# Optimization experiments

Hardware: AMD Instinct MI355X
Metric: run time of the kernel (lower is better)

Reference implementation:

```python
import jax, jax.numpy as jnp
import numpy as np

VOCAB, EMB, HID, SEQ, BATCH, NLAYERS = 10000, 512, 1024, 128, 64, 2


def setup_inputs() -> dict:
    key = jax.random.key(0)
    ks = jax.random.split(key, 10)
    b = 1.0 / np.sqrt(HID)
    U = lambda k, shape, a: jax.random.uniform(k, shape, jnp.float32, -a, a)
    return {
        "inputs": jax.random.randint(ks[0], (SEQ, BATCH), 0, VOCAB, dtype=jnp.int32),
        "hidden": jnp.zeros((NLAYERS, BATCH, HID), jnp.float32),
        "emb": U(ks[1], (VOCAB, EMB), 0.1),
        # layer 0: Linear(emb+hid -> hid), split into input/recurrent parts
        "W0x": U(ks[2], (HID, EMB), b),
        "W0h": U(ks[3], (HID, HID), b),
        "b0": U(ks[4], (HID,), b),
        # layer 1: Linear(2*hid -> hid)
        "W1x": U(ks[5], (HID, HID), b),
        "W1h": U(ks[6], (HID, HID), b),
        "b1": U(ks[7], (HID,), b),
        "Wout": U(ks[8], (VOCAB, HID), 0.1),
        "bout": jnp.zeros((VOCAB,), jnp.float32),
    }


def reference(inputs, hidden, emb, W0x, W0h, b0, W1x, W1h, b1, Wout, bout):
    # Stacked tanh RNN; dropout is identity since dp_keep_prob = 1.0.
    def step(h, tok):
        x = emb[tok]  # (B, E)
        h0 = jnp.tanh(x @ W0x.T + h[0] @ W0h.T + b0)   # (B, H)
        h1 = jnp.tanh(h0 @ W1x.T + h[1] @ W1h.T + b1)  # (B, H)
        logits = h1 @ Wout.T + bout                     # (B, V)
        return jnp.stack([h0, h1]), logits

    final_hidden, logits = jax.lax.scan(step, hidden, inputs)
    return logits, final_hidden
```

## Files before the change

kernel.cpp:

```cpp
#include <hip/hip_runtime.h>
#include <hip/hip_bf16.h>

#define SEQ 128
#define BATCH 64
#define EMB 512
#define HID 1024
#define VOCAB 10000
#define NPAD 10240
#define MROWS 8192
#define BH (BATCH * HID)

typedef unsigned short u16;
typedef unsigned int u32;
typedef __attribute__((ext_vector_type(4))) float f32x4;
typedef __attribute__((ext_vector_type(8))) short short8;
typedef __attribute__((ext_vector_type(8))) __bf16 bf16x8;

__device__ __forceinline__ u16 f2bf(float f) {
  u32 u = __builtin_bit_cast(u32, f);
  u = (u + 0x7fffu + ((u >> 16) & 1u)) >> 16;
  return (u16)u;
}
__device__ __forceinline__ float bf2f(u16 h) {
  u32 u = ((u32)h) << 16;
  return __builtin_bit_cast(float, u);
}
__device__ __forceinline__ f32x4 mfma_bf16(short8 a, short8 b, f32x4 c) {
  return __builtin_amdgcn_mfma_f32_16x16x32_bf16(
      __builtin_bit_cast(bf16x8, a), __builtin_bit_cast(bf16x8, b), c, 0, 0, 0);
}
__device__ __forceinline__ void gload16(const u16* g, u16* l) {
  __builtin_amdgcn_global_load_lds(
      (__attribute__((address_space(1))) void*)g,
      (__attribute__((address_space(3))) void*)l, 16, 0, 0);
}

__global__ void k_cvt(const float* __restrict__ s, u16* __restrict__ d, int n) {
  int i = blockIdx.x * 256 + threadIdx.x;
  if (i < n) d[i] = f2bf(s[i]);
}
__global__ void k_cvt_wout(const float* __restrict__ s, u16* __restrict__ d) {
  int i = blockIdx.x * 256 + threadIdx.x;
  if (i < NPAD * HID) {
    int row = i >> 10;
    d[i] = (row < VOCAB) ? f2bf(s[i]) : (u16)0;
  }
}
__global__ void k_gather(const int* __restrict__ toks, const float* __restrict__ emb,
                         u16* __restrict__ X) {
  int i = blockIdx.x * 256 + threadIdx.x;
  if (i < MROWS * EMB) {
    int r = i >> 9, e = i & 511;
    X[i] = f2bf(emb[(size_t)toks[r] * EMB + e]);
  }
}
__global__ void k_zero(int* __restrict__ p, int n) {
  int i = blockIdx.x * 256 + threadIdx.x;
  if (i < n) p[i] = 0;
}

__global__ __launch_bounds__(256) void k_gemm(const u16* __restrict__ A, const u16* __restrict__ B,
                                              float* __restrict__ C, int K, int ldc, int nvalid,
                                              const float* __restrict__ bias) {
  __shared__ u16 As[128 * 32];
  __shared__ u16 Bs[128 * 32];
  const int tid = threadIdx.x, lane = tid & 63, wid = tid >> 6;
  const int wm = wid >> 1, wn = wid & 1;
  const int bm = blockIdx.x, bn = blockIdx.y;
  const int r4 = tid >> 2;
  const int csw = (((tid & 3) ^ ((r4 >> 1) & 3))) * 8;
  f32x4 acc[4][4] = {};
  const u16* Ab = A + (size_t)bm * 128 * K;
  const u16* Bb = B + (size_t)bn * 128 * K;
  const int nkt = K >> 5;
  for (int kt = 0; kt < nkt; ++kt) {
    const int k0 = kt * 32;
    __syncthreads();
#pragma unroll
    for (int c = 0; c < 2; ++c) {
      gload16(Ab + (size_t)(c * 64 + r4) * K + k0 + csw, &As[c * 2048 + wid * 512]);
      gload16(Bb + (size_t)(c * 64 + r4) * K + k0 + csw, &Bs[c * 2048 + wid * 512]);
    }
    __syncthreads();
    short8 af[4], bf[4];
    const int rr = lane & 15, g = lane >> 4;
    const int kq2 = ((g ^ ((rr >> 1) & 3))) * 8;
#pragma unroll
    for (int mi = 0; mi < 4; ++mi) af[mi] = *(const short8*)&As[(wm * 64 + mi * 16 + rr) * 32 + kq2];
#pragma unroll
    for (int ni = 0; ni < 4; ++ni) bf[ni] = *(const short8*)&Bs[(wn * 64 + ni * 16 + rr) * 32 + kq2];
#pragma unroll
    for (int mi = 0; mi < 4; ++mi)
#pragma unroll
      for (int ni = 0; ni < 4; ++ni) acc[mi][ni] = mfma_bf16(af[mi], bf[ni], acc[mi][ni]);
  }
#pragma unroll
  for (int mi = 0; mi < 4; ++mi)
#pragma unroll
    for (int ni = 0; ni < 4; ++ni) {
      const int col = bn * 128 + wn * 64 + ni * 16 + (lane & 15);
      if (col < nvalid) {
        const float bb = bias ? bias[col] : 0.0f;
#pragma unroll
        for (int r = 0; r < 4; ++r) {
          const int row = bm * 128 + wm * 64 + mi * 16 + (lane >> 4) * 4 + r;
          C[(size_t)row * ldc + col] = acc[mi][ni][r] + bb;
        }
      }
    }
}

__device__ __forceinline__ void gbar(int* bar, int bid, int step) {
  __syncthreads();
  if (threadIdx.x == 0) {
    __threadfence();
    int a = atomicAdd(&bar[(bid >> 3) * 64], 1);
    if (a == (step + 1) * 8 - 1) {
      int r = atomicAdd(&bar[1024], 1);
      if (r == (step + 1) * 16 - 1)
        __hip_atomic_store(&bar[1088], step + 1, __ATOMIC_RELAXED, __HIP_MEMORY_SCOPE_AGENT);
    }
    while (__hip_atomic_load(&bar[1088], __ATOMIC_RELAXED, __HIP_MEMORY_SCOPE_AGENT) < step + 1)
      __builtin_amdgcn_s_sleep(1);
    __threadfence();
  }
  __syncthreads();
}

template <int NKT>
__device__ __forceinline__ void slab_acc(const u16* __restrict__ A, const u16* __restrict__ Ws,
                                         int kt0, int rowbase, int lane, f32x4* acc) {
  const int rr = lane & 15, g = lane >> 4;
  const u16* ap = A + (size_t)(rowbase + rr) * HID + g * 8;
  const int sw = rr & 7;
#pragma unroll
  for (int i = 0; i < NKT; ++i) {
    const int kt = kt0 + i;
    short8 af = *(const short8*)(ap + kt * 32);
    short8 bf = *(const short8*)&Ws[rr * 1024 + (((kt * 4 + g) ^ sw) * 8)];
    *acc = mfma_bf16(af, bf, *acc);
  }
}

__global__ __launch_bounds__(512) void k_rnn(const u16* __restrict__ W0h,
                                             const u16* __restrict__ W1x,
                                             const u16* __restrict__ W1h,
                                             const float* __restrict__ pre0,
                                             const float* __restrict__ b0,
                                             const float* __restrict__ b1, u16* __restrict__ H0all,
                                             u16* __restrict__ H1all, const u16* __restrict__ Zb,
                                             int* __restrict__ bar) {
  __shared__ u16 Wl[2][16 * 1024];
  __shared__ float Pf[64][20];
  const int bid = blockIdx.x;
  const bool is_h1 = bid < 64;
  const int c0 = (bid & 63) * 16;
  const int tid = threadIdx.x, lane = tid & 63, wid = tid >> 6;
  const int rr = lane & 15, g = lane >> 4;
  const int rowbase = (wid & 3) * 16;

  {
    const u16* Wa = is_h1 ? W1x : W0h;
#pragma unroll
    for (int i = 0; i < 4; ++i) {
      int ch = tid + i * 512, row = ch >> 7, c = ch & 127, sc = c ^ (row & 7);
      *(short8*)&Wl[0][row * 1024 + sc * 8] = *(const short8*)&Wa[(size_t)(c0 + row) * HID + c * 8];
      if (is_h1)
        *(short8*)&Wl[1][row * 1024 + sc * 8] =
            *(const short8*)&W1h[(size_t)(c0 + row) * HID + c * 8];
    }
  }
  __syncthreads();

  const float bb = (is_h1 ? b1 : b0)[c0 + rr];
  const int col = c0 + rr;
  const int orow = rowbase + g * 4;

  {
    f32x4 acc = {};
    if (!is_h1) {
      slab_acc<16>(Zb, &Wl[0][0], (wid < 4) ? 0 : 16, rowbase, lane, &acc);
      if (wid >= 4)
#pragma unroll
        for (int r = 0; r < 4; ++r) Pf[orow + r][rr] = acc[r];
    }
    __syncthreads();
    if (!is_h1 && wid < 4)
#pragma unroll
      for (int r = 0; r < 4; ++r)
        H0all[(orow + r) * HID + col] =
            f2bf(tanhf(acc[r] + Pf[orow + r][rr] + pre0[(orow + r) * HID + col] + bb));
  }
  gbar(bar, bid, 0);

  for (int t = 0; t < SEQ; ++t) {
    if (is_h1) {
      f32x4 acc = {};
      if (wid < 4) {
        slab_acc<32>(H0all + (size_t)t * BH, &Wl[0][0], 0, rowbase, lane, &acc);
      } else {
        const u16* A2 = t ? (H1all + (size_t)(t - 1) * BH) : (Zb + BH);
        slab_acc<32>(A2, &Wl[1][0], 0, rowbase, lane, &acc);
#pragma unroll
        for (int r = 0; r < 4; ++r) Pf[orow + r][rr] = acc[r];
      }
      __syncthreads();
      if (wid < 4) {
        u16* out = H1all + (size_t)t * BH;
#pragma unroll
        for (int r = 0; r < 4; ++r)
          out[(orow + r) * HID + col] = f2bf(tanhf(acc[r] + Pf[orow + r][rr] + bb));
      }
    } else {
      f32x4 acc = {};
      const bool live = t < SEQ - 1;
      if (live) {
        slab_acc<16>(H0all + (size_t)t * BH, &Wl[0][0], (wid < 4) ? 0 : 16, rowbase, lane, &acc);
        if (wid >= 4)
#pragma unroll
          for (int r = 0; r < 4; ++r) Pf[orow + r][rr] = acc[r];
      }
      __syncthreads();
      if (live && wid < 4) {
        const float* ci = pre0 + (size_t)(t + 1) * BH;
        u16* out = H0all + (size_t)(t + 1) * BH;
#pragma unroll
        for (int r = 0; r < 4; ++r)
          out[(orow + r) * HID + col] =
              f2bf(tanhf(acc[r] + Pf[orow + r][rr] + ci[(orow + r) * HID + col] + bb));
      }
    }
    gbar(bar, bid, t + 1);
  }
}

__global__ void k_finalh(const u16* __restrict__ H0all, const u16* __restrict__ H1all,
                         float* __restrict__ out) {
  int i = blockIdx.x * 256 + threadIdx.x;
  if (i < 2 * BH) {
    u16 v = (i < BH) ? H0all[(size_t)(SEQ - 1) * BH + i] : H1all[(size_t)(SEQ - 1) * BH + (i - BH)];
    out[(size_t)MROWS * VOCAB + i] = bf2f(v);
  }
}

extern "C" void kernel_launch(void* const* d_in, const int* in_sizes, int n_in, void* d_out,
                              int out_size, void* d_ws, size_t ws_size, hipStream_t stream) {
  (void)in_sizes; (void)n_in; (void)out_size; (void)ws_size;
  const int* toks = (const int*)d_in[0];
  const float* hid0 = (const float*)d_in[1];
  const float* emb = (const float*)d_in[2];
  const float* W0x = (const float*)d_in[3];
  const float* W0h = (const float*)d_in[4];
  const float* b0 = (const float*)d_in[5];
  const float* W1x = (const float*)d_in[6];
  const float* W1h = (const float*)d_in[7];
  const float* b1 = (const float*)d_in[8];
  const float* Wout = (const float*)d_in[9];
  const float* bout = (const float*)d_in[10];
  float* out = (float*)d_out;

  char* ws = (char*)d_ws;
  u16* Xb = (u16*)(ws);
  u16* W0xb = (u16*)(ws + 8388608);
  u16* W0hb = (u16*)(ws + 9437184);
  u16* W1xb = (u16*)(ws + 11534336);
  u16* W1hb = (u16*)(ws + 13631488);
  u16* Woutb = (u16*)(ws + 15728640);
  float* pre0 = (float*)(ws + 36700160);
  u16* H0all = (u16*)(ws + 70254592);
  u16* H1all = (u16*)(ws + 87031808);
  u16* Zb = (u16*)(ws + 103809024);
  int* bar = (int*)(ws + 104071168);

  auto g = [](int n) { return dim3((unsigned)((n + 255) / 256)); };
  k_zero<<<g(1152), 256, 0, stream>>>(bar, 1152);
  k_cvt<<<g(HID * EMB), 256, 0, stream>>>(W0x, W0xb, HID * EMB);
  k_cvt<<<g(HID * HID), 256, 0, stream>>>(W0h, W0hb, HID * HID);
  k_cvt<<<g(HID * HID), 256, 0, stream>>>(W1x, W1xb, HID * HID);
  k_cvt<<<g(HID * HID), 256, 0, stream>>>(W1h, W1hb, HID * HID);
  k_cvt<<<g(2 * BH), 256, 0, stream>>>(hid0, Zb, 2 * BH);
  k_cvt_wout<<<g(NPAD * HID), 256, 0, stream>>>(Wout, Woutb);
  k_gather<<<g(MROWS * EMB), 256, 0, stream>>>(toks, emb, Xb);

  k_gemm<<<dim3(MROWS / 128, HID / 128), 256, 0, stream>>>(Xb, W0xb, pre0, EMB, HID, HID, nullptr);

  {
    void* args[] = {(void*)&W0hb, (void*)&W1xb, (void*)&W1hb, (void*)&pre0, (void*)&b0,
                    (void*)&b1,   (void*)&H0all, (void*)&H1all, (void*)&Zb, (void*)&bar};
    hipLaunchCooperativeKernel((const void*)k_rnn, dim3(128), dim3(512), args, 0, stream);
  }

  k_gemm<<<dim3(MROWS / 128, NPAD / 128), 256, 0, stream>>>(H1all, Woutb, out, HID, VOCAB, VOCAB,
                                                            bout);
  k_finalh<<<g(2 * BH), 256, 0, stream>>>(H0all, H1all, out);
}
```

Before: 2.395 ms.

## Streamline recurrent grid barrier, prefetch A fragments and pre0, use coherent stores

Replaces the fence-based grid barrier with a cheaper scheme. Hidden-state outputs are written with system-coherent stores (sc0 sc1), each thread waits on its own vmcnt, the two __threadfence calls and the separate release flag are dropped, and waiters poll the second-level counter directly. It also loads all A fragments up front in slab_acc and prefetches the pre0 input-projection values before the matmul, to hide global-load latency on the serial recurrent critical path. The barrier's correctness now rests on store-cache bypass instead of fences, and more blocks poll one shared counter, which may add contention.

```diff
diff --git a/kernel.cpp b/kernel.cpp
--- a/kernel.cpp
+++ b/kernel.cpp
@@ -33,6 +33,9 @@
   __builtin_amdgcn_global_load_lds(
       (__attribute__((address_space(1))) void*)g,
       (__attribute__((address_space(3))) void*)l, 16, 0, 0);
+}
+__device__ __forceinline__ void st_ic(u16* p, u16 v) {
+  asm volatile("global_store_short %0, %1, off sc0 sc1" ::"v"(p), "v"((u32)v) : "memory");
 }
 
 __global__ void k_cvt(const float* __restrict__ s, u16* __restrict__ d, int n) {
@@ -111,18 +114,14 @@
 }
 
 __device__ __forceinline__ void gbar(int* bar, int bid, int step) {
+  asm volatile("s_waitcnt vmcnt(0)" ::: "memory");
   __syncthreads();
   if (threadIdx.x == 0) {
-    __threadfence();
     int a = atomicAdd(&bar[(bid >> 3) * 64], 1);
-    if (a == (step + 1) * 8 - 1) {
-      int r = atomicAdd(&bar[1024], 1);
-      if (r == (step + 1) * 16 - 1)
-        __hip_atomic_store(&bar[1088], step + 1, __ATOMIC_RELAXED, __HIP_MEMORY_SCOPE_AGENT);
-    }
-    while (__hip_atomic_load(&bar[1088], __ATOMIC_RELAXED, __HIP_MEMORY_SCOPE_AGENT) < step + 1)
-      __builtin_amdgcn_s_sleep(1);
-    __threadfence();
+    if (a == (step + 1) * 8 - 1) atomicAdd(&bar[1024], 1);
+    const int tgt = (step + 1) * 16;
+    while (__hip_atomic_load(&bar[1024], __ATOMIC_RELAXED, __HIP_MEMORY_SCOPE_AGENT) < tgt)
+      __builtin_amdgcn_s_sleep(2);
   }
   __syncthreads();
 }
@@ -133,12 +132,14 @@
   const int rr = lane & 15, g = lane >> 4;
   const u16* ap = A + (size_t)(rowbase + rr) * HID + g * 8;
   const int sw = rr & 7;
+  short8 af[NKT];
+#pragma unroll
+  for (int i = 0; i < NKT; ++i) af[i] = *(const short8*)(ap + (size_t)(kt0 + i) * 32);
 #pragma unroll
   for (int i = 0; i < NKT; ++i) {
     const int kt = kt0 + i;
-    short8 af = *(const short8*)(ap + kt * 32);
     short8 bf = *(const short8*)&Ws[rr * 1024 + (((kt * 4 + g) ^ sw) * 8)];
-    *acc = mfma_bf16(af, bf, *acc);
+    *acc = mfma_bf16(af[i], bf, *acc);
   }
 }
 
@@ -179,17 +180,21 @@
   {
     f32x4 acc = {};
     if (!is_h1) {
+      float civ[4];
+#pragma unroll
+      for (int r = 0; r < 4; ++r) civ[r] = pre0[(orow + r) * HID + col];
       slab_acc<16>(Zb, &Wl[0][0], (wid < 4) ? 0 : 16, rowbase, lane, &acc);
       if (wid >= 4)
 #pragma unroll
         for (int r = 0; r < 4; ++r) Pf[orow + r][rr] = acc[r];
-    }
-    __syncthreads();
-    if (!is_h1 && wid < 4)
-#pragma unroll
-      for (int r = 0; r < 4; ++r)
-        H0all[(orow + r) * HID + col] =
-            f2bf(tanhf(acc[r] + Pf[orow + r][rr] + pre0[(orow + r) * HID + col] + bb));
+      __syncthreads();
+      if (wid < 4)
+#pragma unroll
+        for (int r = 0; r < 4; ++r)
+          st_ic(&H0all[(orow + r) * HID + col], f2bf(tanhf(acc[r] + Pf[orow + r][rr] + civ[r] + bb)));
+    } else {
+      __syncthreads();
+    }
   }
   gbar(bar, bid, 0);
 
@@ -209,12 +214,16 @@
         u16* out = H1all + (size_t)t * BH;
 #pragma unroll
         for (int r = 0; r < 4; ++r)
-          out[(orow + r) * HID + col] = f2bf(tanhf(acc[r] + Pf[orow + r][rr] + bb));
+          st_ic(&out[(orow + r) * HID + col], f2bf(tanhf(acc[r] + Pf[orow + r][rr] + bb)));
       }
     } else {
       f32x4 acc = {};
       const bool live = t < SEQ - 1;
+      float civ[4];
       if (live) {
+        const float* ci = pre0 + (size_t)(t + 1) * BH;
+#pragma unroll
+        for (int r = 0; r < 4; ++r) civ[r] = ci[(orow + r) * HID + col];
         slab_acc<16>(H0all + (size_t)t * BH, &Wl[0][0], (wid < 4) ? 0 : 16, rowbase, lane, &acc);
         if (wid >= 4)
 #pragma unroll
@@ -222,12 +231,10 @@
       }
       __syncthreads();
       if (live && wid < 4) {
-        const float* ci = pre0 + (size_t)(t + 1) * BH;
         u16* out = H0all + (size_t)(t + 1) * BH;
 #pragma unroll
         for (int r = 0; r < 4; ++r)
-          out[(orow + r) * HID + col] =
-              f2bf(tanhf(acc[r] + Pf[orow + r][rr] + ci[(orow + r) * HID + col] + bb));
+          st_ic(&out[(orow + r) * HID + col], f2bf(tanhf(acc[r] + Pf[orow + r][rr] + civ[r] + bb)));
       }
     }
     gbar(bar, bid, t + 1);
```

Measured after the change: 2.027 ms. -15.4%, faster.
